# Optimization experiments

Hardware: AMD Instinct MI355X
Metric: run time of the kernel (lower is better)

The kernel has to match this reference:

```python
import jax, jax.numpy as jnp
import numpy as np

N = 50000      # nodes
E = 800000     # edges (avg degree 16)
IN = 256       # in_size
HID = 64       # hid_size
H = 4          # n_head
OUT = 64       # out_size


def setup_inputs() -> dict:
    key = jax.random.key(0)
    ks = jax.random.split(key, 16)
    g = lambda k, shp: jax.random.normal(k, shp, jnp.float32) * 0.1
    return {
        "features": jax.random.normal(ks[0], (N, IN), jnp.float32),
        "src": jax.random.randint(ks[1], (E,), 0, N, jnp.int32),
        "dst": jax.random.randint(ks[2], (E,), 0, N, jnp.int32),
        # layer 0: 256 -> 4 heads x 64
        "W0": g(ks[3], (IN, H * HID)), "al0": g(ks[4], (H, HID)), "ar0": g(ks[5], (H, HID)), "b0": g(ks[6], (H * HID,)),
        # layer 1: 256 -> 4 heads x 64
        "W1": g(ks[7], (H * HID, H * HID)), "al1": g(ks[8], (H, HID)), "ar1": g(ks[9], (H, HID)), "b1": g(ks[10], (H * HID,)),
        # layer 2: 256 -> 4 heads x 64, relu activation, mean over heads
        "W2": g(ks[11], (H * HID, H * OUT)), "al2": g(ks[12], (H, OUT)), "ar2": g(ks[13], (H, OUT)), "b2": g(ks[14], (H * OUT,)),
    }


def gat_conv(h, src, dst, W, al, ar, b, apply_relu):
    """DGL GATConv (eval mode, dropout off), residual identity since in == H*D."""
    n = h.shape[0]
    hh, dd = al.shape
    feat = (h @ W).reshape(n, hh, dd)                       # [N,H,D]
    el = jnp.einsum('nhd,hd->nh', feat, al)                 # [N,H]
    er = jnp.einsum('nhd,hd->nh', feat, ar)                 # [N,H]
    e = jax.nn.leaky_relu(el[src] + er[dst], negative_slope=0.2)  # [E,H]
    # segment softmax over incoming edges of each dst node
    m = jax.ops.segment_max(e, dst, num_segments=n)         # [N,H]
    ex = jnp.exp(e - m[dst])
    den = jax.ops.segment_sum(ex, dst, num_segments=n)      # [N,H]
    alpha = ex / den[dst]                                   # [E,H]
    rst = jax.ops.segment_sum(feat[src] * alpha[..., None], dst, num_segments=n)  # [N,H,D]
    rst = rst + h.reshape(n, hh, dd) + b.reshape(1, hh, dd)  # residual + bias
    return jax.nn.relu(rst) if apply_relu else rst


def reference(features, src, dst, W0, al0, ar0, b0, W1, al1, ar1, b1, W2, al2, ar2, b2):
    h = gat_conv(features, src, dst, W0, al0, ar0, b0, False).reshape(N, -1)
    h = gat_conv(h, src, dst, W1, al1, ar1, b1, False).reshape(N, -1)
    h = gat_conv(h, src, dst, W2, al2, ar2, b2, True).mean(axis=1)  # [N,OUT]
    return h
```

## Files before the change

### kernel.cpp

```cpp
#include <hip/hip_runtime.h>

#define NNODE 50000
#define NEDGE 800000
#define NH 4
#define DH 64
#define HD 256
#define PADN 50048
#define EPAD 64

typedef __attribute__((ext_vector_type(8))) short short8v;
typedef __attribute__((ext_vector_type(4))) float float4v;

static __device__ __forceinline__ float b2f(unsigned short u) {
  union { float f; unsigned v; } x; x.v = ((unsigned)u) << 16; return x.f;
}
static __device__ __forceinline__ unsigned short f2b(float f) {
  unsigned u = __builtin_bit_cast(unsigned, f);
  u += 0x7fff + ((u >> 16) & 1);
  return (unsigned short)(u >> 16);
}

__global__ __launch_bounds__(256) void k_cvtw(const float* __restrict__ W0,
                                              const float* __restrict__ W1,
                                              const float* __restrict__ W2,
                                              unsigned short* __restrict__ T0,
                                              unsigned short* __restrict__ T1,
                                              unsigned short* __restrict__ T2) {
  const float* W = blockIdx.y == 0 ? W0 : (blockIdx.y == 1 ? W1 : W2);
  unsigned short* T = blockIdx.y == 0 ? T0 : (blockIdx.y == 1 ? T1 : T2);
  int k = blockIdx.x;
  int nn = threadIdx.x;
  T[nn * HD + k] = f2b(W[k * HD + nn]);
}

__global__ __launch_bounds__(256) void k_mkfrag(const unsigned short* __restrict__ Wt0,
                                                const unsigned short* __restrict__ Wt1,
                                                const unsigned short* __restrict__ Wt2,
                                                unsigned short* __restrict__ F0,
                                                unsigned short* __restrict__ F1,
                                                unsigned short* __restrict__ F2) {
  int L = blockIdx.y;
  const unsigned short* Wt = L == 0 ? Wt0 : (L == 1 ? Wt1 : Wt2);
  unsigned short* F = L == 0 ? F0 : (L == 1 ? F1 : F2);
  int idx = blockIdx.x * 256 + threadIdx.x;
  int lane = idx & 63;
  int ni = (idx >> 6) & 3;
  int head = (idx >> 8) & 3;
  int t = idx >> 10;
  short8v v = *(const short8v*)(Wt + (size_t)(head * 64 + ni * 16 + (lane & 15)) * HD +
                                t * 32 + (lane >> 4) * 8);
  *(short8v*)(F + (size_t)idx * 8) = v;
}

__global__ __launch_bounds__(256) void k_wal(const float* __restrict__ W0,
                                             const float* __restrict__ W1,
                                             const float* __restrict__ W2,
                                             const float* __restrict__ al0,
                                             const float* __restrict__ ar0,
                                             const float* __restrict__ al1,
                                             const float* __restrict__ ar1,
                                             const float* __restrict__ al2,
                                             const float* __restrict__ ar2,
                                             unsigned short* __restrict__ F0,
                                             unsigned short* __restrict__ F1,
                                             unsigned short* __restrict__ F2) {
  int L = blockIdx.y;
  const float* W = L == 0 ? W0 : (L == 1 ? W1 : W2);
  const float* al = L == 0 ? al0 : (L == 1 ? al1 : al2);
  const float* ar = L == 0 ? ar0 : (L == 1 ? ar1 : ar2);
  unsigned short* F = L == 0 ? F0 : (L == 1 ? F1 : F2);
  int k = threadIdx.x;
  const float* wr = W + k * HD;
  float s[8] = {};
#pragma unroll 4
  for (int h = 0; h < 4; ++h)
    for (int d = 0; d < 64; ++d) {
      float wv = wr[h * 64 + d];
      s[h] = fmaf(wv, al[h * 64 + d], s[h]);
      s[4 + h] = fmaf(wv, ar[h * 64 + d], s[4 + h]);
    }
  int base = (k >> 5) * 512 + ((k >> 3) & 3) * 128 + (k & 7);
#pragma unroll
  for (int j = 0; j < 8; ++j) F[base + j * 8] = f2b(s[j]);
#pragma unroll
  for (int j = 8; j < 16; ++j) F[base + j * 8] = 0;
}

__global__ void k_edge(const int* __restrict__ src, const int* __restrict__ dst,
                       int* __restrict__ fill, int* __restrict__ csrp) {
  int e = blockIdx.x * 256 + threadIdx.x;
  if (e < NEDGE) {
    int d = dst[e];
    int pos = atomicAdd(&fill[d], 1);
    if (pos < EPAD) csrp[(d << 6) + pos] = src[e];
  }
}

template <bool FP32A>
__global__ __launch_bounds__(256) void k_gemm(const float* __restrict__ Af,
                                              const unsigned short* __restrict__ Ab,
                                              const unsigned short* __restrict__ Wtf,
                                              const unsigned short* __restrict__ walrf,
                                              unsigned short* __restrict__ featb,
                                              float* __restrict__ el,
                                              float* __restrict__ er) {
  __shared__ unsigned short As[8][64][40];
  const int row0 = blockIdx.x * 64;
  const int tid = threadIdx.x;
  const int lane = tid & 63;
  const int head = tid >> 6;
  const int lr = lane & 15;
  const int kf = (lane >> 4) * 8;

  {
    const int r = tid >> 2, c = tid & 3;
    int grow = row0 + r;
    if (FP32A) {
      int gr = grow < NNODE ? grow : 0;
      const float* ap = Af + (size_t)gr * HD + c * 8;
#pragma unroll
      for (int t = 0; t < 8; ++t) {
        float4v f0 = *(const float4v*)(ap + t * 32);
        float4v f1 = *(const float4v*)(ap + t * 32 + 4);
        uint4 pk;
        pk.x = (unsigned)f2b(f0.x) | ((unsigned)f2b(f0.y) << 16);
        pk.y = (unsigned)f2b(f0.z) | ((unsigned)f2b(f0.w) << 16);
        pk.z = (unsigned)f2b(f1.x) | ((unsigned)f2b(f1.y) << 16);
        pk.w = (unsigned)f2b(f1.z) | ((unsigned)f2b(f1.w) << 16);
        *(uint4*)&As[t][r][c * 8] = pk;
      }
    } else {
      const unsigned short* ap = Ab + (size_t)grow * HD + c * 8;
#pragma unroll
      for (int t = 0; t < 8; ++t)
        *(uint4*)&As[t][r][c * 8] = *(const uint4*)(ap + t * 32);
    }
  }
  __syncthreads();

  float4v acc[4][4] = {};
  float4v acc_e = {};

#pragma unroll 2
  for (int t = 0; t < 8; ++t) {
    short8v af[4], bfr[4], bfe;
#pragma unroll
    for (int ni = 0; ni < 4; ++ni)
      bfr[ni] = *(const short8v*)(Wtf + ((size_t)(((t * 4 + head) * 4 + ni) * 64 + lane)) * 8);
    bfe = *(const short8v*)(walrf + (size_t)(t * 64 + lane) * 8);
#pragma unroll
    for (int mi = 0; mi < 4; ++mi)
      af[mi] = *(const short8v*)&As[t][mi * 16 + lr][kf];
#pragma unroll
    for (int mi = 0; mi < 4; ++mi)
#pragma unroll
      for (int ni = 0; ni < 4; ++ni)
        acc[mi][ni] = __builtin_amdgcn_mfma_f32_16x16x32_bf16(bfr[ni], af[mi], acc[mi][ni], 0, 0, 0);
    acc_e = __builtin_amdgcn_mfma_f32_16x16x32_bf16(af[head], bfe, acc_e, 0, 0, 0);
  }

  const int rg = (lane >> 4) * 4;

#pragma unroll
  for (int mi = 0; mi < 4; ++mi) {
    int node = row0 + mi * 16 + lr;
    if (node < NNODE) {
#pragma unroll
      for (int ni = 0; ni < 4; ++ni) {
        uint2 o;
        o.x = (unsigned)f2b(acc[mi][ni][0]) | ((unsigned)f2b(acc[mi][ni][1]) << 16);
        o.y = (unsigned)f2b(acc[mi][ni][2]) | ((unsigned)f2b(acc[mi][ni][3]) << 16);
        *(uint2*)(featb + (size_t)node * HD + head * 64 + ni * 16 + rg) = o;
      }
    }
  }

#pragma unroll
  for (int reg = 0; reg < 4; ++reg) {
    int grow = row0 + head * 16 + rg + reg;
    if (grow < NNODE) {
      if (lr < 4) el[grow * NH + lr] = acc_e[reg];
      else if (lr < 8) er[grow * NH + lr - 4] = acc_e[reg];
    }
  }
}

template <int LAYER>
__global__ __launch_bounds__(256) void k_agg(const int* __restrict__ fillarr,
                                             const int* __restrict__ csrp,
                                             const float* __restrict__ el,
                                             const float* __restrict__ er,
                                             const unsigned short* __restrict__ featb,
                                             const unsigned short* __restrict__ hinb,
                                             const float* __restrict__ hinf,
                                             const float* __restrict__ bias,
                                             void* __restrict__ outv) {
  const int tid = threadIdx.x;
  const int w = tid >> 6;
  const int lane = tid & 63;
  const int n = blockIdx.x * 4 + w;
  const int e2 = lane >> 5;
  const int h = (lane >> 3) & 3;
  const int dg = lane & 7;
  const int deg = min(fillarr[n], EPAD);

  __shared__ float alpha_s[4][64][4];
  __shared__ int src_s[4][64];

  const float4v er4 = *(const float4v*)(er + n * 4);

  int s = 0;
  float4v lg = {-1e30f, -1e30f, -1e30f, -1e30f};
  if (lane < deg) {
    s = csrp[(n << 6) + lane];
    float4v e4 = *(const float4v*)(el + s * 4);
#pragma unroll
    for (int c = 0; c < 4; ++c) {
      float x = e4[c] + er4[c];
      lg[c] = x > 0.f ? x : 0.2f * x;
    }
  }
  float4v p;
#pragma unroll
  for (int c = 0; c < 4; ++c) p[c] = __expf(lg[c]);
  *(float4v*)&alpha_s[w][lane][0] = p;
  src_s[w][lane] = s;

  float4v denp = p;
#pragma unroll
  for (int off = 32; off; off >>= 1)
#pragma unroll
    for (int c = 0; c < 4; ++c) denp[c] += __shfl_xor(denp[c], off, 64);

  float acc[8] = {};
  const int foff = (h << 6) + (dg << 3);
  int nit = (((deg + 1) >> 1) + 3) & ~3;
  for (int pj = 0; pj < nit; pj += 4) {
    float a[4];
    int sv[4];
    uint4 u[4];
#pragma unroll
    for (int q = 0; q < 4; ++q) {
      int e = ((pj + q) << 1) + e2;
      a[q] = alpha_s[w][e][h];
      sv[q] = src_s[w][e];
    }
#pragma unroll
    for (int q = 0; q < 4; ++q)
      u[q] = *(const uint4*)(featb + ((size_t)sv[q] << 8) + foff);
#pragma unroll
    for (int q = 0; q < 4; ++q) {
      unsigned uu[4] = {u[q].x, u[q].y, u[q].z, u[q].w};
#pragma unroll
      for (int t = 0; t < 4; ++t) {
        float flo = __builtin_bit_cast(float, uu[t] << 16);
        float fhi = __builtin_bit_cast(float, uu[t] & 0xffff0000u);
        acc[2 * t] = fmaf(a[q], flo, acc[2 * t]);
        acc[2 * t + 1] = fmaf(a[q], fhi, acc[2 * t + 1]);
      }
    }
  }
#pragma unroll
  for (int k = 0; k < 8; ++k) acc[k] += __shfl_xor(acc[k], 32, 64);

  float dh = h == 0 ? denp[0] : (h == 1 ? denp[1] : (h == 2 ? denp[2] : denp[3]));
  float inv = dh > 0.f ? 1.f / dh : 0.f;

  float hr[8];
  if (LAYER == 0) {
    const float4v* hp = (const float4v*)(hinf + ((size_t)n << 8) + foff);
    float4v h0 = hp[0], h1 = hp[1];
    hr[0] = h0.x; hr[1] = h0.y; hr[2] = h0.z; hr[3] = h0.w;
    hr[4] = h1.x; hr[5] = h1.y; hr[6] = h1.z; hr[7] = h1.w;
  } else {
    uint4 hv = *(const uint4*)(hinb + ((size_t)n << 8) + foff);
    unsigned hh[4] = {hv.x, hv.y, hv.z, hv.w};
#pragma unroll
    for (int k = 0; k < 8; ++k) {
      unsigned hu = (k & 1) ? (hh[k >> 1] & 0xffff0000u) : (hh[k >> 1] << 16);
      hr[k] = __builtin_bit_cast(float, hu);
    }
  }
  const float4v* bp = (const float4v*)(bias + foff);
  float4v bb0 = bp[0], bb1 = bp[1];
  float bb[8] = {bb0.x, bb0.y, bb0.z, bb0.w, bb1.x, bb1.y, bb1.z, bb1.w};
  float v[8];
#pragma unroll
  for (int k = 0; k < 8; ++k) v[k] = acc[k] * inv + hr[k] + bb[k];

  if (LAYER == 2) {
#pragma unroll
    for (int k = 0; k < 8; ++k) {
      v[k] = fmaxf(v[k], 0.f);
      v[k] += __shfl_xor(v[k], 8, 64);
      v[k] += __shfl_xor(v[k], 16, 64);
      v[k] *= 0.25f;
    }
    if (lane < 8) {
      float* out = (float*)outv + (size_t)n * DH + (dg << 3);
      *(float4v*)out = (float4v){v[0], v[1], v[2], v[3]};
      *(float4v*)(out + 4) = (float4v){v[4], v[5], v[6], v[7]};
    }
  } else {
    if (e2 == 0) {
      uint4 o;
      unsigned ov[4];
#pragma unroll
      for (int q = 0; q < 4; ++q)
        ov[q] = (unsigned)f2b(v[2 * q]) | ((unsigned)f2b(v[2 * q + 1]) << 16);
      o.x = ov[0]; o.y = ov[1]; o.z = ov[2]; o.w = ov[3];
      *(uint4*)((unsigned short*)outv + ((size_t)n << 8) + foff) = o;
    }
  }
}

extern "C" void kernel_launch(void* const* d_in, const int* in_sizes, int n_in,
                              void* d_out, int out_size, void* d_ws, size_t ws_size,
                              hipStream_t stream) {
  const float* features = (const float*)d_in[0];
  const int* src = (const int*)d_in[1];
  const int* dst = (const int*)d_in[2];
  const float* W0 = (const float*)d_in[3];
  const float* al0 = (const float*)d_in[4];
  const float* ar0 = (const float*)d_in[5];
  const float* b0 = (const float*)d_in[6];
  const float* W1 = (const float*)d_in[7];
  const float* al1 = (const float*)d_in[8];
  const float* ar1 = (const float*)d_in[9];
  const float* b1 = (const float*)d_in[10];
  const float* W2 = (const float*)d_in[11];
  const float* al2 = (const float*)d_in[12];
  const float* ar2 = (const float*)d_in[13];
  const float* b2 = (const float*)d_in[14];
  float* out = (float*)d_out;

  char* p = (char*)d_ws;
  auto carve = [&](size_t bytes) {
    char* q = p;
    p += (bytes + 255) & ~(size_t)255;
    return q;
  };
  unsigned short* h1b = (unsigned short*)carve((size_t)PADN * HD * 2);
  unsigned short* h2b = (unsigned short*)carve((size_t)PADN * HD * 2);
  unsigned short* featb = (unsigned short*)carve((size_t)PADN * HD * 2);
  unsigned short* wt0 = (unsigned short*)carve((size_t)HD * HD * 2);
  unsigned short* wt1 = (unsigned short*)carve((size_t)HD * HD * 2);
  unsigned short* wt2 = (unsigned short*)carve((size_t)HD * HD * 2);
  unsigned short* wtf0 = (unsigned short*)carve((size_t)8192 * 8 * 2);
  unsigned short* wtf1 = (unsigned short*)carve((size_t)8192 * 8 * 2);
  unsigned short* wtf2 = (unsigned short*)carve((size_t)8192 * 8 * 2);
  unsigned short* walf0 = (unsigned short*)carve((size_t)8 * 512 * 2);
  unsigned short* walf1 = (unsigned short*)carve((size_t)8 * 512 * 2);
  unsigned short* walf2 = (unsigned short*)carve((size_t)8 * 512 * 2);
  float* el = (float*)carve((size_t)NNODE * NH * 4);
  float* er = (float*)carve((size_t)NNODE * NH * 4);
  int* fill = (int*)carve((size_t)NNODE * 4);
  int* csrp = (int*)carve((size_t)NNODE * EPAD * 4);

  hipMemsetAsync(fill, 0, (size_t)NNODE * 4, stream);

  k_cvtw<<<dim3(HD, 3), 256, 0, stream>>>(W0, W1, W2, wt0, wt1, wt2);
  k_mkfrag<<<dim3(32, 3), 256, 0, stream>>>(wt0, wt1, wt2, wtf0, wtf1, wtf2);
  k_wal<<<dim3(1, 3), 256, 0, stream>>>(W0, W1, W2, al0, ar0, al1, ar1, al2, ar2,
                                        walf0, walf1, walf2);
  k_edge<<<NEDGE / 256, 256, 0, stream>>>(src, dst, fill, csrp);

  dim3 gg(PADN / 64);

  k_gemm<true><<<gg, 256, 0, stream>>>(features, nullptr, wtf0, walf0, featb, el, er);
  k_agg<0><<<NNODE / 4, 256, 0, stream>>>(fill, csrp, el, er, featb, nullptr, features, b0, h1b);

  k_gemm<false><<<gg, 256, 0, stream>>>(nullptr, h1b, wtf1, walf1, featb, el, er);
  k_agg<1><<<NNODE / 4, 256, 0, stream>>>(fill, csrp, el, er, featb, h1b, nullptr, b1, h2b);

  k_gemm<false><<<gg, 256, 0, stream>>>(nullptr, h2b, wtf2, walf2, featb, el, er);
  k_agg<2><<<NNODE / 4, 256, 0, stream>>>(fill, csrp, el, er, featb, h2b, nullptr, b2, (void*)out);
}
```

Measured before the change: 383.2 us.

## Halve GEMM row tile, fuse weight prep kernels, compute softmax denominator in loop

New measurement: 363.8 us. -5.1%, faster.

```diff
diff --git a/kernel.cpp b/kernel.cpp
--- a/kernel.cpp
+++ b/kernel.cpp
@@ -20,36 +20,26 @@
   return (unsigned short)(u >> 16);
 }
 
-__global__ __launch_bounds__(256) void k_cvtw(const float* __restrict__ W0,
-                                              const float* __restrict__ W1,
-                                              const float* __restrict__ W2,
-                                              unsigned short* __restrict__ T0,
-                                              unsigned short* __restrict__ T1,
-                                              unsigned short* __restrict__ T2) {
-  const float* W = blockIdx.y == 0 ? W0 : (blockIdx.y == 1 ? W1 : W2);
-  unsigned short* T = blockIdx.y == 0 ? T0 : (blockIdx.y == 1 ? T1 : T2);
-  int k = blockIdx.x;
-  int nn = threadIdx.x;
-  T[nn * HD + k] = f2b(W[k * HD + nn]);
-}
-
-__global__ __launch_bounds__(256) void k_mkfrag(const unsigned short* __restrict__ Wt0,
-                                                const unsigned short* __restrict__ Wt1,
-                                                const unsigned short* __restrict__ Wt2,
+__global__ __launch_bounds__(256) void k_mkfrag(const float* __restrict__ W0,
+                                                const float* __restrict__ W1,
+                                                const float* __restrict__ W2,
                                                 unsigned short* __restrict__ F0,
                                                 unsigned short* __restrict__ F1,
                                                 unsigned short* __restrict__ F2) {
   int L = blockIdx.y;
-  const unsigned short* Wt = L == 0 ? Wt0 : (L == 1 ? Wt1 : Wt2);
+  const float* W = L == 0 ? W0 : (L == 1 ? W1 : W2);
   unsigned short* F = L == 0 ? F0 : (L == 1 ? F1 : F2);
   int idx = blockIdx.x * 256 + threadIdx.x;
   int lane = idx & 63;
   int ni = (idx >> 6) & 3;
   int head = (idx >> 8) & 3;
   int t = idx >> 10;
-  short8v v = *(const short8v*)(Wt + (size_t)(head * 64 + ni * 16 + (lane & 15)) * HD +
-                                t * 32 + (lane >> 4) * 8);
-  *(short8v*)(F + (size_t)idx * 8) = v;
+  int row = head * 64 + ni * 16 + (lane & 15);
+  int kb = t * 32 + (lane >> 4) * 8;
+  unsigned short v[8];
+#pragma unroll
+  for (int j = 0; j < 8; ++j) v[j] = f2b(W[(size_t)(kb + j) * HD + row]);
+  *(short8v*)(F + (size_t)idx * 8) = *(const short8v*)v;
 }
 
 __global__ __launch_bounds__(256) void k_wal(const float* __restrict__ W0,
@@ -70,14 +60,20 @@
   const float* ar = L == 0 ? ar0 : (L == 1 ? ar1 : ar2);
   unsigned short* F = L == 0 ? F0 : (L == 1 ? F1 : F2);
   int k = threadIdx.x;
-  const float* wr = W + k * HD;
+  const float* wr = W + (size_t)k * HD;
   float s[8] = {};
+#pragma unroll
+  for (int h = 0; h < 4; ++h)
 #pragma unroll 4
-  for (int h = 0; h < 4; ++h)
-    for (int d = 0; d < 64; ++d) {
-      float wv = wr[h * 64 + d];
-      s[h] = fmaf(wv, al[h * 64 + d], s[h]);
-      s[4 + h] = fmaf(wv, ar[h * 64 + d], s[4 + h]);
+    for (int dq = 0; dq < 16; ++dq) {
+      float4v w4 = *(const float4v*)(wr + h * 64 + dq * 4);
+      const float* alp = al + h * 64 + dq * 4;
+      const float* arp = ar + h * 64 + dq * 4;
+#pragma unroll
+      for (int j = 0; j < 4; ++j) {
+        s[h] = fmaf(w4[j], alp[j], s[h]);
+        s[4 + h] = fmaf(w4[j], arp[j], s[4 + h]);
+      }
     }
   int base = (k >> 5) * 512 + ((k >> 3) & 3) * 128 + (k & 7);
 #pragma unroll
@@ -104,8 +100,8 @@
                                               unsigned short* __restrict__ featb,
                                               float* __restrict__ el,
                                               float* __restrict__ er) {
-  __shared__ unsigned short As[8][64][40];
-  const int row0 = blockIdx.x * 64;
+  __shared__ unsigned short As[8][32][40];
+  const int row0 = blockIdx.x * 32;
   const int tid = threadIdx.x;
   const int lane = tid & 63;
   const int head = tid >> 6;
@@ -113,56 +109,53 @@
   const int kf = (lane >> 4) * 8;
 
   {
-    const int r = tid >> 2, c = tid & 3;
+    const int r = tid >> 3, c = tid & 7;
     int grow = row0 + r;
     if (FP32A) {
       int gr = grow < NNODE ? grow : 0;
-      const float* ap = Af + (size_t)gr * HD + c * 8;
+      const float* ap = Af + (size_t)gr * HD + c * 4;
 #pragma unroll
       for (int t = 0; t < 8; ++t) {
-        float4v f0 = *(const float4v*)(ap + t * 32);
-        float4v f1 = *(const float4v*)(ap + t * 32 + 4);
-        uint4 pk;
-        pk.x = (unsigned)f2b(f0.x) | ((unsigned)f2b(f0.y) << 16);
-        pk.y = (unsigned)f2b(f0.z) | ((unsigned)f2b(f0.w) << 16);
-        pk.z = (unsigned)f2b(f1.x) | ((unsigned)f2b(f1.y) << 16);
-        pk.w = (unsigned)f2b(f1.z) | ((unsigned)f2b(f1.w) << 16);
-        *(uint4*)&As[t][r][c * 8] = pk;
+        float4v f = *(const float4v*)(ap + t * 32);
+        uint2 pk;
+        pk.x = (unsigned)f2b(f.x) | ((unsigned)f2b(f.y) << 16);
+        pk.y = (unsigned)f2b(f.z) | ((unsigned)f2b(f.w) << 16);
+        *(uint2*)&As[t][r][c * 4] = pk;
       }
     } else {
-      const unsigned short* ap = Ab + (size_t)grow * HD + c * 8;
+      const unsigned short* ap = Ab + (size_t)grow * HD + c * 4;
 #pragma unroll
       for (int t = 0; t < 8; ++t)
-        *(uint4*)&As[t][r][c * 8] = *(const uint4*)(ap + t * 32);
+        *(uint2*)&As[t][r][c * 4] = *(const uint2*)(ap + t * 32);
     }
   }
   __syncthreads();
 
-  float4v acc[4][4] = {};
+  float4v acc[2][4] = {};
   float4v acc_e = {};
 
 #pragma unroll 2
   for (int t = 0; t < 8; ++t) {
-    short8v af[4], bfr[4], bfe;
+    short8v af[2], bfr[4], bfe;
 #pragma unroll
     for (int ni = 0; ni < 4; ++ni)
       bfr[ni] = *(const short8v*)(Wtf + ((size_t)(((t * 4 + head) * 4 + ni) * 64 + lane)) * 8);
     bfe = *(const short8v*)(walrf + (size_t)(t * 64 + lane) * 8);
 #pragma unroll
-    for (int mi = 0; mi < 4; ++mi)
+    for (int mi = 0; mi < 2; ++mi)
       af[mi] = *(const short8v*)&As[t][mi * 16 + lr][kf];
 #pragma unroll
-    for (int mi = 0; mi < 4; ++mi)
+    for (int mi = 0; mi < 2; ++mi)
 #pragma unroll
       for (int ni = 0; ni < 4; ++ni)
         acc[mi][ni] = __builtin_amdgcn_mfma_f32_16x16x32_bf16(bfr[ni], af[mi], acc[mi][ni], 0, 0, 0);
-    acc_e = __builtin_amdgcn_mfma_f32_16x16x32_bf16(af[head], bfe, acc_e, 0, 0, 0);
+    acc_e = __builtin_amdgcn_mfma_f32_16x16x32_bf16(af[head & 1], bfe, acc_e, 0, 0, 0);
   }
 
   const int rg = (lane >> 4) * 4;
 
 #pragma unroll
-  for (int mi = 0; mi < 4; ++mi) {
+  for (int mi = 0; mi < 2; ++mi) {
     int node = row0 + mi * 16 + lr;
     if (node < NNODE) {
 #pragma unroll
@@ -177,8 +170,8 @@
 
 #pragma unroll
   for (int reg = 0; reg < 4; ++reg) {
-    int grow = row0 + head * 16 + rg + reg;
-    if (grow < NNODE) {
+    int grow = row0 + (head & 1) * 16 + rg + reg;
+    if (head < 2 && grow < NNODE) {
       if (lr < 4) el[grow * NH + lr] = acc_e[reg];
       else if (lr < 8) er[grow * NH + lr - 4] = acc_e[reg];
     }
@@ -226,13 +219,8 @@
   *(float4v*)&alpha_s[w][lane][0] = p;
   src_s[w][lane] = s;
 
-  float4v denp = p;
-#pragma unroll
-  for (int off = 32; off; off >>= 1)
-#pragma unroll
-    for (int c = 0; c < 4; ++c) denp[c] += __shfl_xor(denp[c], off, 64);
-
   float acc[8] = {};
+  float aden = 0.f;
   const int foff = (h << 6) + (dg << 3);
   int nit = (((deg + 1) >> 1) + 3) & ~3;
   for (int pj = 0; pj < nit; pj += 4) {
@@ -250,6 +238,7 @@
       u[q] = *(const uint4*)(featb + ((size_t)sv[q] << 8) + foff);
 #pragma unroll
     for (int q = 0; q < 4; ++q) {
+      aden += a[q];
       unsigned uu[4] = {u[q].x, u[q].y, u[q].z, u[q].w};
 #pragma unroll
       for (int t = 0; t < 4; ++t) {
@@ -262,9 +251,9 @@
   }
 #pragma unroll
   for (int k = 0; k < 8; ++k) acc[k] += __shfl_xor(acc[k], 32, 64);
-
-  float dh = h == 0 ? denp[0] : (h == 1 ? denp[1] : (h == 2 ? denp[2] : denp[3]));
-  float inv = dh > 0.f ? 1.f / dh : 0.f;
+  aden += __shfl_xor(aden, 32, 64);
+
+  float inv = aden > 0.f ? 1.f / aden : 0.f;
 
   float hr[8];
   if (LAYER == 0) {
@@ -343,9 +332,6 @@
   unsigned short* h1b = (unsigned short*)carve((size_t)PADN * HD * 2);
   unsigned short* h2b = (unsigned short*)carve((size_t)PADN * HD * 2);
   unsigned short* featb = (unsigned short*)carve((size_t)PADN * HD * 2);
-  unsigned short* wt0 = (unsigned short*)carve((size_t)HD * HD * 2);
-  unsigned short* wt1 = (unsigned short*)carve((size_t)HD * HD * 2);
-  unsigned short* wt2 = (unsigned short*)carve((size_t)HD * HD * 2);
   unsigned short* wtf0 = (unsigned short*)carve((size_t)8192 * 8 * 2);
   unsigned short* wtf1 = (unsigned short*)carve((size_t)8192 * 8 * 2);
   unsigned short* wtf2 = (unsigned short*)carve((size_t)8192 * 8 * 2);
@@ -359,13 +345,12 @@
 
   hipMemsetAsync(fill, 0, (size_t)NNODE * 4, stream);
 
-  k_cvtw<<<dim3(HD, 3), 256, 0, stream>>>(W0, W1, W2, wt0, wt1, wt2);
-  k_mkfrag<<<dim3(32, 3), 256, 0, stream>>>(wt0, wt1, wt2, wtf0, wtf1, wtf2);
+  k_mkfrag<<<dim3(32, 3), 256, 0, stream>>>(W0, W1, W2, wtf0, wtf1, wtf2);
   k_wal<<<dim3(1, 3), 256, 0, stream>>>(W0, W1, W2, al0, ar0, al1, ar1, al2, ar2,
                                         walf0, walf1, walf2);
   k_edge<<<NEDGE / 256, 256, 0, stream>>>(src, dst, fill, csrp);
 
-  dim3 gg(PADN / 64);
+  dim3 gg(PADN / 32);
 
   k_gemm<true><<<gg, 256, 0, stream>>>(features, nullptr, wtf0, walf0, featb, el, er);
   k_agg<0><<<NNODE / 4, 256, 0, stream>>>(fill, csrp, el, er, featb, nullptr, features, b0, h1b);
```
